# Optimization experiments

Measured on AMD Instinct MI355X. Metric: run time of the kernel, lower is better.

## Reference

```python
import jax, jax.numpy as jnp
import numpy as np

N_NODES = 100000
N_EDGES = 1600000
IN_FEATS = 128
HIDDEN = 128
NUM_CLASSES = 64


def setup_inputs() -> dict:
    key = jax.random.key(0)
    k1, k2, k3, k4, k5 = jax.random.split(key, 5)
    inputs = jax.random.normal(k1, (N_NODES, IN_FEATS), dtype=jnp.float32)
    src = jax.random.randint(k2, (N_EDGES,), 0, N_NODES, dtype=jnp.int32)
    dst = jax.random.randint(k3, (N_EDGES,), 0, N_NODES, dtype=jnp.int32)
    W1 = jax.random.normal(k4, (IN_FEATS, HIDDEN), dtype=jnp.float32) / np.sqrt(IN_FEATS)
    b1 = jnp.zeros((HIDDEN,), dtype=jnp.float32)
    W2 = jax.random.normal(k5, (HIDDEN, NUM_CLASSES), dtype=jnp.float32) / np.sqrt(HIDDEN)
    b2 = jnp.zeros((NUM_CLASSES,), dtype=jnp.float32)
    return {"inputs": inputs, "src": src, "dst": dst, "W1": W1, "b1": b1, "W2": W2, "b2": b2}


def _graph_conv(x, src, dst, W, b, n_nodes):
    # DGL GraphConv, norm='both': h = D_in^{-1/2} A D_out^{-1/2} x W + b
    ones = jnp.ones(src.shape[0], dtype=x.dtype)
    deg_out = jax.ops.segment_sum(ones, src, num_segments=n_nodes)
    deg_in = jax.ops.segment_sum(ones, dst, num_segments=n_nodes)
    norm_src = jax.lax.rsqrt(jnp.clip(deg_out, 1.0))  # [N]
    norm_dst = jax.lax.rsqrt(jnp.clip(deg_in, 1.0))   # [N]
    x = x * norm_src[:, None]
    msgs = x[src]                                      # [E, d] gather
    agg = jax.ops.segment_sum(msgs, dst, num_segments=n_nodes)  # [N, d] scatter-add
    agg = agg * norm_dst[:, None]
    return agg @ W + b


def reference(inputs, src, dst, W1, b1, W2, b2):
    n = inputs.shape[0]
    h = _graph_conv(inputs, src, dst, W1, b1, n)
    h = jax.nn.relu(h)
    h = _graph_conv(h, src, dst, W2, b2, n)
    return h
```

## Files before the change

kernel.cpp:

```cpp
#include <hip/hip_runtime.h>
#include <hip/hip_bf16.h>

#define N_FEATS_IN 128
#define BK_BITS 8
#define BK_SIZE 256
#define EPB 4096
#define MAXNB 512

typedef _Float16 h8 __attribute__((ext_vector_type(8)));
typedef float    f4v __attribute__((ext_vector_type(4)));
typedef float    f8v __attribute__((ext_vector_type(8)));

__device__ inline int wave_incl_scan(int v) {
    const int lane = threadIdx.x & 63;
    for (int off = 1; off < 64; off <<= 1) {
        int u = __shfl_up(v, off, 64);
        if (lane >= off) v += u;
    }
    return v;
}

__device__ inline int block_excl_scan(int s, int* ws, int* total) {
    const int lane = threadIdx.x & 63, wid = threadIdx.x >> 6;
    int inc = wave_incl_scan(s);
    if (lane == 63) ws[wid] = inc;
    __syncthreads();
    int woff = 0;
#pragma unroll
    for (int w = 0; w < 4; ++w) woff += (w < wid) ? ws[w] : 0;
    if (total) *total = ws[0] + ws[1] + ws[2] + ws[3];
    return woff + inc - s;
}

__global__ __launch_bounds__(256) void hist_kernel(
    const int* __restrict__ src, const int* __restrict__ dst,
    int* __restrict__ bh_d, int* __restrict__ bh_s,
    const float* __restrict__ W1, const float* __restrict__ W2,
    _Float16* __restrict__ wf1g, _Float16* __restrict__ wf2g,
    int E, int NB) {
    __shared__ int hd[MAXNB];
    __shared__ int hs[MAXNB];
    const int t = threadIdx.x;

    const int widx = blockIdx.x * 256 + t;
    if (widx < 128 * 128) {
        const int i = widx;
        const int k = i >> 7, c = i & 127;
        const int tt = c >> 4, s = k >> 5, q = (k >> 3) & 3, j = k & 7;
        wf1g[(((tt * 4 + s) * 4 + q) * 16 + (c & 15)) * 8 + j] =
            (_Float16)W1[i];
    } else if (widx < 128 * 128 + 128 * 64) {
        const int i = widx - 128 * 128;
        const int k = i >> 6, c = i & 63;
        const int tt = c >> 4, s = k >> 5, q = (k >> 3) & 3, j = k & 7;
        wf2g[(((tt * 4 + s) * 4 + q) * 16 + (c & 15)) * 8 + j] =
            (_Float16)W2[i];
    }

    for (int i = t; i < NB; i += 256) { hd[i] = 0; hs[i] = 0; }
    __syncthreads();
    const int base = blockIdx.x * EPB;
    const int end = min(base + EPB, E);
    for (int e = base + t; e < end; e += 256) {
        atomicAdd(&hd[dst[e] >> BK_BITS], 1);
        atomicAdd(&hs[src[e] >> BK_BITS], 1);
    }
    __syncthreads();
    for (int i = t; i < NB; i += 256) {
        bh_d[(size_t)blockIdx.x * NB + i] = hd[i];
        bh_s[(size_t)blockIdx.x * NB + i] = hs[i];
    }
}

__global__ __launch_bounds__(256) void colprefix2_kernel(
    int* __restrict__ bh_d, int* __restrict__ bh_s,
    int* __restrict__ tot_d, int* __restrict__ tot_s, int NBLK, int NB) {
    __shared__ int ws[4];
    const int b = blockIdx.x;
    const int t = threadIdx.x;
    int carry = 0;
    for (int base = 0; base < NBLK; base += 256) {
        const int r = base + t;
        const int v = (r < NBLK) ? bh_d[(size_t)r * NB + b] : 0;
        int total;
        const int e = block_excl_scan(v, ws, &total);
        if (r < NBLK) bh_d[(size_t)r * NB + b] = carry + e;
        carry += total;
        __syncthreads();
    }
    if (t == 0) tot_d[b] = carry;
    carry = 0;
    for (int base = 0; base < NBLK; base += 256) {
        const int r = base + t;
        const int v = (r < NBLK) ? bh_s[(size_t)r * NB + b] : 0;
        int total;
        const int e = block_excl_scan(v, ws, &total);
        if (r < NBLK) bh_s[(size_t)r * NB + b] = carry + e;
        carry += total;
        __syncthreads();
    }
    if (t == 0) tot_s[b] = carry;
}

__global__ __launch_bounds__(256) void bscan2_kernel(
    const int* __restrict__ tot_d, const int* __restrict__ tot_s,
    int* __restrict__ gb_d, int* __restrict__ gb_s,
    int* __restrict__ row_ptr, int NB, int N, int E) {
    __shared__ int ws[4];
    const int t = threadIdx.x;
    {
        const int a = (2 * t < NB) ? tot_d[2 * t] : 0;
        const int b = (2 * t + 1 < NB) ? tot_d[2 * t + 1] : 0;
        const int excl = block_excl_scan(a + b, ws, nullptr);
        if (2 * t < NB) gb_d[2 * t] = excl;
        if (2 * t + 1 < NB) gb_d[2 * t + 1] = excl + a;
    }
    __syncthreads();
    {
        const int a = (2 * t < NB) ? tot_s[2 * t] : 0;
        const int b = (2 * t + 1 < NB) ? tot_s[2 * t + 1] : 0;
        const int excl = block_excl_scan(a + b, ws, nullptr);
        if (2 * t < NB) gb_s[2 * t] = excl;
        if (2 * t + 1 < NB) gb_s[2 * t + 1] = excl + a;
    }
    if (t == 0) { gb_d[NB] = E; gb_s[NB] = E; row_ptr[N] = E; }
}

__global__ __launch_bounds__(256) void scatter2_kernel(
    const int* __restrict__ src, const int* __restrict__ dst,
    const int* __restrict__ bh_d, const int* __restrict__ bh_s,
    const int* __restrict__ gb_d, const int* __restrict__ gb_s,
    unsigned int* __restrict__ ebuf, unsigned char* __restrict__ sbuf,
    int E, int NB) {
    __shared__ int cd[MAXNB];
    __shared__ int cs[MAXNB];
    const int t = threadIdx.x;
    for (int i = t; i < NB; i += 256) {
        cd[i] = bh_d[(size_t)blockIdx.x * NB + i] + gb_d[i];
        cs[i] = bh_s[(size_t)blockIdx.x * NB + i] + gb_s[i];
    }
    __syncthreads();
    const int base = blockIdx.x * EPB;
    const int end = min(base + EPB, E);
    for (int e = base + t; e < end; e += 256) {
        const int d = dst[e];
        const int s = src[e];
        const int pd = atomicAdd(&cd[d >> BK_BITS], 1);
        ebuf[pd] = ((unsigned)s << 8) | (unsigned)(d & (BK_SIZE - 1));
        const int ps = atomicAdd(&cs[s >> BK_BITS], 1);
        sbuf[ps] = (unsigned char)(s & (BK_SIZE - 1));
    }
}

__global__ __launch_bounds__(256) void bucket_csr_kernel(
    const unsigned int* __restrict__ ebuf, const int* __restrict__ gb_d,
    const unsigned char* __restrict__ sbuf, const int* __restrict__ gb_s,
    int* __restrict__ row_ptr, float* __restrict__ norm_dst,
    float* __restrict__ norm_src, int* __restrict__ edge_src, int N) {
    __shared__ int cnt[BK_SIZE];
    __shared__ int lro[BK_SIZE];
    __shared__ int ws[4];
    const int b = blockIdx.x;
    const int t = threadIdx.x;
    const int beg = gb_d[b], end = gb_d[b + 1];
    const int node = b * BK_SIZE + t;

    cnt[t] = 0;
    __syncthreads();
    for (int j = beg + t; j < end; j += 256)
        atomicAdd(&cnt[ebuf[j] & (BK_SIZE - 1)], 1);
    __syncthreads();

    const int v = cnt[t];
    const int excl = block_excl_scan(v, ws, nullptr);
    lro[t] = beg + excl;
    if (node < N) {
        row_ptr[node] = beg + excl;
        norm_dst[node] = rsqrtf(fmaxf((float)v, 1.0f));
    }
    __syncthreads();
    cnt[t] = 0;
    __syncthreads();

    for (int j = beg + t; j < end; j += 256) {
        const unsigned int ed = ebuf[j];
        const int dl = ed & (BK_SIZE - 1);
        const int p = atomicAdd(&cnt[dl], 1);
        edge_src[lro[dl] + p] = (int)(ed >> 8);
    }

    __syncthreads();
    cnt[t] = 0;
    __syncthreads();
    const int sb = gb_s[b], se = gb_s[b + 1];
    for (int j = sb + t; j < se; j += 256)
        atomicAdd(&cnt[sbuf[j]], 1);
    __syncthreads();
    if (node < N)
        norm_src[node] = rsqrtf(fmaxf((float)cnt[t], 1.0f));
}

template <int OC, bool XHALF>
__global__ __launch_bounds__(256) void mfma_gemm_kernel(
    const void* __restrict__ Xv, const _Float16* __restrict__ Wg,
    const float* __restrict__ scale, _Float16* __restrict__ Y, int n) {
    constexpr int K = 128;
    constexpr int NT = OC / 16;
    constexpr int RPB = 128;
    __shared__ _Float16 Wf[NT * 4 * 64 * 8];

    const int tid = threadIdx.x;
    for (int i = tid * 8; i < K * OC; i += 256 * 8)
        *(h8*)&Wf[i] = *(const h8*)&Wg[i];
    __syncthreads();

    const int lane = tid & 63;
    const int wv = tid >> 6;
    const int m = lane & 15, q = lane >> 4;

#pragma unroll
    for (int it = 0; it < RPB / 64; ++it) {
        const int rbase = blockIdx.x * RPB + it * 64 + wv * 16;
        const int lrow = min(rbase + m, n - 1);

        h8 a[4];
        if constexpr (XHALF) {
            const _Float16* X = (const _Float16*)Xv;
            const _Float16* p = &X[(size_t)lrow * K + q * 8];
#pragma unroll
            for (int s = 0; s < 4; ++s) a[s] = *(const h8*)(p + s * 32);
        } else {
            const float* X = (const float*)Xv;
            const float* p = &X[(size_t)lrow * K + q * 8];
#pragma unroll
            for (int s = 0; s < 4; ++s) {
                const float4 u0 = *(const float4*)(p + s * 32);
                const float4 u1 = *(const float4*)(p + s * 32 + 4);
                h8 v;
                v[0] = (_Float16)u0.x; v[1] = (_Float16)u0.y;
                v[2] = (_Float16)u0.z; v[3] = (_Float16)u0.w;
                v[4] = (_Float16)u1.x; v[5] = (_Float16)u1.y;
                v[6] = (_Float16)u1.z; v[7] = (_Float16)u1.w;
                a[s] = v;
            }
        }

        f4v acc[NT];
#pragma unroll
        for (int t = 0; t < NT; ++t) acc[t] = (f4v)0.0f;

#pragma unroll
        for (int s = 0; s < 4; ++s) {
#pragma unroll
            for (int t = 0; t < NT; ++t) {
                const h8 b = *(const h8*)&Wf[((t * 4 + s) * 64 + lane) * 8];
                acc[t] = __builtin_amdgcn_mfma_f32_16x16x32_f16(
                    a[s], b, acc[t], 0, 0, 0);
            }
        }

#pragma unroll
        for (int r = 0; r < 4; ++r) {
            const int orow = rbase + q * 4 + r;
            if (orow < n) {
                const float sc = scale[orow];
#pragma unroll
                for (int t = 0; t < NT; ++t)
                    Y[(size_t)orow * OC + t * 16 + m] =
                        (_Float16)(acc[t][r] * sc);
            }
        }
    }
}

template <int FEAT, bool RELU, bool OUT_HALF>
__global__ __launch_bounds__(256) void gather_agg_kernel(
    const _Float16* __restrict__ T, const int* __restrict__ row_ptr,
    const int* __restrict__ edge_src, const float* __restrict__ norm_dst,
    const float* __restrict__ bias, void* __restrict__ outv, int n) {
    constexpr int TPN = FEAT / 8;
    constexpr int NPB = 256 / TPN;
    const int node = blockIdx.x * NPB + threadIdx.x / TPN;
    const int f8 = threadIdx.x % TPN;
    if (node >= n) return;
    const int beg = row_ptr[node];
    const int end = row_ptr[node + 1];
    const h8* T8 = (const h8*)T;

    f8v acc = (f8v)0.0f;
    int j = beg;
    for (; j + 7 < end; j += 8) {
        int s[8];
#pragma unroll
        for (int u = 0; u < 8; ++u) s[u] = edge_src[j + u];
        h8 a[8];
#pragma unroll
        for (int u = 0; u < 8; ++u) a[u] = T8[(size_t)s[u] * TPN + f8];
#pragma unroll
        for (int u = 0; u < 8; ++u)
            acc += __builtin_convertvector(a[u], f8v);
    }
    for (; j + 3 < end; j += 4) {
        int s[4];
#pragma unroll
        for (int u = 0; u < 4; ++u) s[u] = edge_src[j + u];
        h8 a[4];
#pragma unroll
        for (int u = 0; u < 4; ++u) a[u] = T8[(size_t)s[u] * TPN + f8];
#pragma unroll
        for (int u = 0; u < 4; ++u)
            acc += __builtin_convertvector(a[u], f8v);
    }
    for (; j < end; ++j)
        acc += __builtin_convertvector(T8[(size_t)edge_src[j] * TPN + f8], f8v);

    const float nd = norm_dst[node];
    float r[8];
#pragma unroll
    for (int k = 0; k < 8; ++k) {
        r[k] = acc[k] * nd + bias[f8 * 8 + k];
        if constexpr (RELU) r[k] = fmaxf(r[k], 0.0f);
    }

    if constexpr (OUT_HALF) {
        _Float16* out = (_Float16*)outv;
        h8 o;
#pragma unroll
        for (int k = 0; k < 8; ++k) o[k] = (_Float16)r[k];
        *(h8*)&out[(size_t)node * FEAT + f8 * 8] = o;
    } else {
        float* out = (float*)outv;
        float4 o0 = make_float4(r[0], r[1], r[2], r[3]);
        float4 o1 = make_float4(r[4], r[5], r[6], r[7]);
        *(float4*)&out[(size_t)node * FEAT + f8 * 8] = o0;
        *(float4*)&out[(size_t)node * FEAT + f8 * 8 + 4] = o1;
    }
}

template <int FEAT, int OC>
__global__ __launch_bounds__(256) void gather_gemm_kernel(
    const _Float16* __restrict__ T, const int* __restrict__ row_ptr,
    const int* __restrict__ edge_src, const float* __restrict__ norm_dst,
    const float* __restrict__ norm_src, const float* __restrict__ bias,
    const _Float16* __restrict__ Wg, _Float16* __restrict__ Y, int n) {
    constexpr int TPN = FEAT / 8;
    constexpr int NPB = 256 / TPN;
    constexpr int AP = FEAT + 8;
    __shared__ _Float16 Ah[NPB * AP];

    const int tid = threadIdx.x;
    const int node = blockIdx.x * NPB + tid / TPN;
    const int f8 = tid % TPN;
    const int nl = tid / TPN;
    const h8* T8 = (const h8*)T;

    float r[8];
    if (node < n) {
        const int beg = row_ptr[node];
        const int end = row_ptr[node + 1];
        f8v acc = (f8v)0.0f;
        int j = beg;
        for (; j + 7 < end; j += 8) {
            int s[8];
#pragma unroll
            for (int u = 0; u < 8; ++u) s[u] = edge_src[j + u];
            h8 a[8];
#pragma unroll
            for (int u = 0; u < 8; ++u) a[u] = T8[(size_t)s[u] * TPN + f8];
#pragma unroll
            for (int u = 0; u < 8; ++u)
                acc += __builtin_convertvector(a[u], f8v);
        }
        for (; j + 3 < end; j += 4) {
            int s[4];
#pragma unroll
            for (int u = 0; u < 4; ++u) s[u] = edge_src[j + u];
            h8 a[4];
#pragma unroll
            for (int u = 0; u < 4; ++u) a[u] = T8[(size_t)s[u] * TPN + f8];
#pragma unroll
            for (int u = 0; u < 4; ++u)
                acc += __builtin_convertvector(a[u], f8v);
        }
        for (; j < end; ++j)
            acc += __builtin_convertvector(T8[(size_t)edge_src[j] * TPN + f8],
                                           f8v);

        const float nd = norm_dst[node];
        const float ns = norm_src[node];
#pragma unroll
        for (int k = 0; k < 8; ++k) {
            float v = acc[k] * nd + bias[f8 * 8 + k];
            v = fmaxf(v, 0.0f);
            r[k] = v * ns;
        }
    } else {
#pragma unroll
        for (int k = 0; k < 8; ++k) r[k] = 0.0f;
    }

    {
        h8 av;
#pragma unroll
        for (int k = 0; k < 8; ++k) av[k] = (_Float16)r[k];
        *(h8*)&Ah[nl * AP + f8 * 8] = av;
    }
    __syncthreads();

    const int lane = tid & 63, w = tid >> 6;
    const int m = lane & 15, q = lane >> 4;
    f4v acc2 = (f4v)0.0f;
#pragma unroll
    for (int s = 0; s < 4; ++s) {
        const h8 a = *(const h8*)&Ah[m * AP + s * 32 + q * 8];
        const h8 b = *(const h8*)&Wg[((w * 4 + s) * 64 + lane) * 8];
        acc2 = __builtin_amdgcn_mfma_f32_16x16x32_f16(a, b, acc2, 0, 0, 0);
    }
#pragma unroll
    for (int rr = 0; rr < 4; ++rr) {
        const int orow = blockIdx.x * NPB + q * 4 + rr;
        if (orow < n)
            Y[(size_t)orow * OC + w * 16 + m] = (_Float16)acc2[rr];
    }
}

extern "C" void kernel_launch(void* const* d_in, const int* in_sizes, int n_in,
                              void* d_out, int out_size, void* d_ws, size_t ws_size,
                              hipStream_t stream) {
    const float* x   = (const float*)d_in[0];
    const int*   src = (const int*)d_in[1];
    const int*   dst = (const int*)d_in[2];
    const float* W1  = (const float*)d_in[3];
    const float* b1  = (const float*)d_in[4];
    const float* W2  = (const float*)d_in[5];
    const float* b2  = (const float*)d_in[6];
    float* out = (float*)d_out;

    const int N = in_sizes[0] / N_FEATS_IN;
    const int E = in_sizes[1];
    const int NB = (N + BK_SIZE - 1) / BK_SIZE;
    const int NBLK = (E + EPB - 1) / EPB;

    auto align4 = [](size_t w) { return (w + 3) & ~(size_t)3; };
    char* base = (char*)d_ws;
    size_t off = 0;
    auto take = [&](size_t words) {
        char* p = base + off * 4;
        off = align4(off + words);
        return p;
    };
    int*   tot_d    = (int*)take(NB);
    int*   tot_s    = (int*)take(NB);
    int*   gb_d     = (int*)take(NB + 1);
    int*   gb_s     = (int*)take(NB + 1);
    int*   bh_d     = (int*)take((size_t)NBLK * NB);
    int*   bh_s     = (int*)take((size_t)NBLK * NB);
    unsigned int*  ebuf = (unsigned int*)take(E);
    unsigned char* sbuf = (unsigned char*)take((E + 3) / 4);
    int*   row_ptr  = (int*)take(N + 1);
    int*   edge_src = (int*)take(E);
    float* norms    = (float*)take(2 * (size_t)N);
    _Float16* t1    = (_Float16*)take((size_t)N * 64);
    _Float16* t2    = (_Float16*)take((size_t)N * 32);
    _Float16* wf1g  = (_Float16*)take(128 * 128 / 2);
    _Float16* wf2g  = (_Float16*)take(128 * 64 / 2);
    float* norm_src = norms;
    float* norm_dst = norms + N;

    hist_kernel<<<NBLK, 256, 0, stream>>>(src, dst, bh_d, bh_s,
                                          W1, W2, wf1g, wf2g, E, NB);
    colprefix2_kernel<<<NB, 256, 0, stream>>>(bh_d, bh_s, tot_d, tot_s,
                                              NBLK, NB);
    bscan2_kernel<<<1, 256, 0, stream>>>(tot_d, tot_s, gb_d, gb_s, row_ptr,
                                         NB, N, E);
    scatter2_kernel<<<NBLK, 256, 0, stream>>>(src, dst, bh_d, bh_s, gb_d, gb_s,
                                              ebuf, sbuf, E, NB);
    bucket_csr_kernel<<<NB, 256, 0, stream>>>(ebuf, gb_d, sbuf, gb_s, row_ptr,
                                              norm_dst, norm_src, edge_src, N);

    mfma_gemm_kernel<128, false><<<(N + 127) / 128, 256, 0, stream>>>(
        x, wf1g, norm_src, t1, N);

    gather_gemm_kernel<128, 64><<<(N + 15) / 16, 256, 0, stream>>>(
        t1, row_ptr, edge_src, norm_dst, norm_src, b1, wf2g, t2, N);

    gather_agg_kernel<64, false, false><<<(N + 31) / 32, 256, 0, stream>>>(
        t2, row_ptr, edge_src, norm_dst, b2, out, N);
}
```

Before: 315.5 us.

## Replace bucketed two-level CSR build with global-atomic degree count and scan

```diff
diff --git a/kernel.cpp b/kernel.cpp
--- a/kernel.cpp
+++ b/kernel.cpp
@@ -2,10 +2,6 @@
 #include <hip/hip_bf16.h>
 
 #define N_FEATS_IN 128
-#define BK_BITS 8
-#define BK_SIZE 256
-#define EPB 4096
-#define MAXNB 512
 
 typedef _Float16 h8 __attribute__((ext_vector_type(8)));
 typedef float    f4v __attribute__((ext_vector_type(4)));
@@ -32,172 +28,97 @@
     return woff + inc - s;
 }
 
-__global__ __launch_bounds__(256) void hist_kernel(
-    const int* __restrict__ src, const int* __restrict__ dst,
-    int* __restrict__ bh_d, int* __restrict__ bh_s,
+__global__ __launch_bounds__(256) void zswz_kernel(
+    int* __restrict__ deg_in, int* __restrict__ deg_out,
     const float* __restrict__ W1, const float* __restrict__ W2,
-    _Float16* __restrict__ wf1g, _Float16* __restrict__ wf2g,
-    int E, int NB) {
-    __shared__ int hd[MAXNB];
-    __shared__ int hs[MAXNB];
-    const int t = threadIdx.x;
-
-    const int widx = blockIdx.x * 256 + t;
-    if (widx < 128 * 128) {
-        const int i = widx;
+    _Float16* __restrict__ wf1g, _Float16* __restrict__ wf2g, int N) {
+    const int g = blockIdx.x * 256 + threadIdx.x;
+    if (g < N) { deg_in[g] = 0; deg_out[g] = 0; }
+    if (g < 128 * 128) {
+        const int i = g;
         const int k = i >> 7, c = i & 127;
         const int tt = c >> 4, s = k >> 5, q = (k >> 3) & 3, j = k & 7;
         wf1g[(((tt * 4 + s) * 4 + q) * 16 + (c & 15)) * 8 + j] =
             (_Float16)W1[i];
-    } else if (widx < 128 * 128 + 128 * 64) {
-        const int i = widx - 128 * 128;
+    } else if (g < 128 * 128 + 128 * 64) {
+        const int i = g - 128 * 128;
         const int k = i >> 6, c = i & 63;
         const int tt = c >> 4, s = k >> 5, q = (k >> 3) & 3, j = k & 7;
         wf2g[(((tt * 4 + s) * 4 + q) * 16 + (c & 15)) * 8 + j] =
             (_Float16)W2[i];
     }
-
-    for (int i = t; i < NB; i += 256) { hd[i] = 0; hs[i] = 0; }
-    __syncthreads();
-    const int base = blockIdx.x * EPB;
-    const int end = min(base + EPB, E);
-    for (int e = base + t; e < end; e += 256) {
-        atomicAdd(&hd[dst[e] >> BK_BITS], 1);
-        atomicAdd(&hs[src[e] >> BK_BITS], 1);
-    }
-    __syncthreads();
-    for (int i = t; i < NB; i += 256) {
-        bh_d[(size_t)blockIdx.x * NB + i] = hd[i];
-        bh_s[(size_t)blockIdx.x * NB + i] = hs[i];
-    }
-}
-
-__global__ __launch_bounds__(256) void colprefix2_kernel(
-    int* __restrict__ bh_d, int* __restrict__ bh_s,
-    int* __restrict__ tot_d, int* __restrict__ tot_s, int NBLK, int NB) {
-    __shared__ int ws[4];
-    const int b = blockIdx.x;
-    const int t = threadIdx.x;
-    int carry = 0;
-    for (int base = 0; base < NBLK; base += 256) {
-        const int r = base + t;
-        const int v = (r < NBLK) ? bh_d[(size_t)r * NB + b] : 0;
-        int total;
-        const int e = block_excl_scan(v, ws, &total);
-        if (r < NBLK) bh_d[(size_t)r * NB + b] = carry + e;
-        carry += total;
-        __syncthreads();
-    }
-    if (t == 0) tot_d[b] = carry;
-    carry = 0;
-    for (int base = 0; base < NBLK; base += 256) {
-        const int r = base + t;
-        const int v = (r < NBLK) ? bh_s[(size_t)r * NB + b] : 0;
-        int total;
-        const int e = block_excl_scan(v, ws, &total);
-        if (r < NBLK) bh_s[(size_t)r * NB + b] = carry + e;
-        carry += total;
-        __syncthreads();
-    }
-    if (t == 0) tot_s[b] = carry;
-}
-
-__global__ __launch_bounds__(256) void bscan2_kernel(
-    const int* __restrict__ tot_d, const int* __restrict__ tot_s,
-    int* __restrict__ gb_d, int* __restrict__ gb_s,
-    int* __restrict__ row_ptr, int NB, int N, int E) {
+}
+
+__global__ __launch_bounds__(256) void deg_kernel(
+    const int* __restrict__ src, const int* __restrict__ dst,
+    int* __restrict__ deg_in, int* __restrict__ deg_out, int E) {
+    const int stride = gridDim.x * 256;
+    for (int e = blockIdx.x * 256 + threadIdx.x; e < E; e += stride) {
+        atomicAdd(&deg_in[dst[e]], 1);
+        atomicAdd(&deg_out[src[e]], 1);
+    }
+}
+
+__global__ __launch_bounds__(256) void scanA_kernel(
+    const int* __restrict__ deg, int* __restrict__ rp,
+    int* __restrict__ part, int N) {
     __shared__ int ws[4];
     const int t = threadIdx.x;
-    {
-        const int a = (2 * t < NB) ? tot_d[2 * t] : 0;
-        const int b = (2 * t + 1 < NB) ? tot_d[2 * t + 1] : 0;
-        const int excl = block_excl_scan(a + b, ws, nullptr);
-        if (2 * t < NB) gb_d[2 * t] = excl;
-        if (2 * t + 1 < NB) gb_d[2 * t + 1] = excl + a;
-    }
-    __syncthreads();
-    {
-        const int a = (2 * t < NB) ? tot_s[2 * t] : 0;
-        const int b = (2 * t + 1 < NB) ? tot_s[2 * t + 1] : 0;
-        const int excl = block_excl_scan(a + b, ws, nullptr);
-        if (2 * t < NB) gb_s[2 * t] = excl;
-        if (2 * t + 1 < NB) gb_s[2 * t + 1] = excl + a;
-    }
-    if (t == 0) { gb_d[NB] = E; gb_s[NB] = E; row_ptr[N] = E; }
-}
-
-__global__ __launch_bounds__(256) void scatter2_kernel(
+    const int i0 = (blockIdx.x * 256 + t) * 4;
+    int d0 = 0, d1 = 0, d2 = 0, d3 = 0;
+    if (i0 + 3 < N) {
+        const int4 v = *(const int4*)&deg[i0];
+        d0 = v.x; d1 = v.y; d2 = v.z; d3 = v.w;
+    } else {
+        if (i0 < N) d0 = deg[i0];
+        if (i0 + 1 < N) d1 = deg[i0 + 1];
+        if (i0 + 2 < N) d2 = deg[i0 + 2];
+        if (i0 + 3 < N) d3 = deg[i0 + 3];
+    }
+    int tot;
+    int r = block_excl_scan(d0 + d1 + d2 + d3, ws, &tot);
+    if (i0 < N) rp[i0] = r; r += d0;
+    if (i0 + 1 < N) rp[i0 + 1] = r; r += d1;
+    if (i0 + 2 < N) rp[i0 + 2] = r; r += d2;
+    if (i0 + 3 < N) rp[i0 + 3] = r;
+    if (t == 0) part[blockIdx.x] = tot;
+}
+
+__global__ __launch_bounds__(256) void scanB_kernel(
+    int* __restrict__ part, int nbs) {
+    __shared__ int ws[4];
+    const int t = threadIdx.x;
+    const int v = (t < nbs) ? part[t] : 0;
+    const int e = block_excl_scan(v, ws, nullptr);
+    if (t < nbs) part[t] = e;
+}
+
+__global__ __launch_bounds__(256) void scanC_kernel(
+    int* __restrict__ rp, int* __restrict__ cur,
+    const int* __restrict__ part,
+    const int* __restrict__ deg_in, const int* __restrict__ deg_out,
+    float* __restrict__ norm_dst, float* __restrict__ norm_src,
+    int N, int E) {
+    const int i = blockIdx.x * 256 + threadIdx.x;
+    if (i < N) {
+        const int r = rp[i] + part[i >> 10];
+        rp[i] = r;
+        cur[i] = r;
+        norm_dst[i] = rsqrtf(fmaxf((float)deg_in[i], 1.0f));
+        norm_src[i] = rsqrtf(fmaxf((float)deg_out[i], 1.0f));
+    }
+    if (i == 0) rp[N] = E;
+}
+
+__global__ __launch_bounds__(256) void scatter_kernel(
     const int* __restrict__ src, const int* __restrict__ dst,
-    const int* __restrict__ bh_d, const int* __restrict__ bh_s,
-    const int* __restrict__ gb_d, const int* __restrict__ gb_s,
-    unsigned int* __restrict__ ebuf, unsigned char* __restrict__ sbuf,
-    int E, int NB) {
-    __shared__ int cd[MAXNB];
-    __shared__ int cs[MAXNB];
-    const int t = threadIdx.x;
-    for (int i = t; i < NB; i += 256) {
-        cd[i] = bh_d[(size_t)blockIdx.x * NB + i] + gb_d[i];
-        cs[i] = bh_s[(size_t)blockIdx.x * NB + i] + gb_s[i];
-    }
-    __syncthreads();
-    const int base = blockIdx.x * EPB;
-    const int end = min(base + EPB, E);
-    for (int e = base + t; e < end; e += 256) {
+    int* __restrict__ cur, int* __restrict__ edge_src, int E) {
+    const int stride = gridDim.x * 256;
+    for (int e = blockIdx.x * 256 + threadIdx.x; e < E; e += stride) {
         const int d = dst[e];
-        const int s = src[e];
-        const int pd = atomicAdd(&cd[d >> BK_BITS], 1);
-        ebuf[pd] = ((unsigned)s << 8) | (unsigned)(d & (BK_SIZE - 1));
-        const int ps = atomicAdd(&cs[s >> BK_BITS], 1);
-        sbuf[ps] = (unsigned char)(s & (BK_SIZE - 1));
-    }
-}
-
-__global__ __launch_bounds__(256) void bucket_csr_kernel(
-    const unsigned int* __restrict__ ebuf, const int* __restrict__ gb_d,
-    const unsigned char* __restrict__ sbuf, const int* __restrict__ gb_s,
-    int* __restrict__ row_ptr, float* __restrict__ norm_dst,
-    float* __restrict__ norm_src, int* __restrict__ edge_src, int N) {
-    __shared__ int cnt[BK_SIZE];
-    __shared__ int lro[BK_SIZE];
-    __shared__ int ws[4];
-    const int b = blockIdx.x;
-    const int t = threadIdx.x;
-    const int beg = gb_d[b], end = gb_d[b + 1];
-    const int node = b * BK_SIZE + t;
-
-    cnt[t] = 0;
-    __syncthreads();
-    for (int j = beg + t; j < end; j += 256)
-        atomicAdd(&cnt[ebuf[j] & (BK_SIZE - 1)], 1);
-    __syncthreads();
-
-    const int v = cnt[t];
-    const int excl = block_excl_scan(v, ws, nullptr);
-    lro[t] = beg + excl;
-    if (node < N) {
-        row_ptr[node] = beg + excl;
-        norm_dst[node] = rsqrtf(fmaxf((float)v, 1.0f));
-    }
-    __syncthreads();
-    cnt[t] = 0;
-    __syncthreads();
-
-    for (int j = beg + t; j < end; j += 256) {
-        const unsigned int ed = ebuf[j];
-        const int dl = ed & (BK_SIZE - 1);
-        const int p = atomicAdd(&cnt[dl], 1);
-        edge_src[lro[dl] + p] = (int)(ed >> 8);
-    }
-
-    __syncthreads();
-    cnt[t] = 0;
-    __syncthreads();
-    const int sb = gb_s[b], se = gb_s[b + 1];
-    for (int j = sb + t; j < se; j += 256)
-        atomicAdd(&cnt[sbuf[j]], 1);
-    __syncthreads();
-    if (node < N)
-        norm_src[node] = rsqrtf(fmaxf((float)cnt[t], 1.0f));
+        const int pos = atomicAdd(&cur[d], 1);
+        edge_src[pos] = src[e];
+    }
 }
 
 template <int OC, bool XHALF>
@@ -438,8 +359,7 @@
 
     const int N = in_sizes[0] / N_FEATS_IN;
     const int E = in_sizes[1];
-    const int NB = (N + BK_SIZE - 1) / BK_SIZE;
-    const int NBLK = (E + EPB - 1) / EPB;
+    const int NBS = (N + 1023) / 1024;
 
     auto align4 = [](size_t w) { return (w + 3) & ~(size_t)3; };
     char* base = (char*)d_ws;
@@ -449,14 +369,10 @@
         off = align4(off + words);
         return p;
     };
-    int*   tot_d    = (int*)take(NB);
-    int*   tot_s    = (int*)take(NB);
-    int*   gb_d     = (int*)take(NB + 1);
-    int*   gb_s     = (int*)take(NB + 1);
-    int*   bh_d     = (int*)take((size_t)NBLK * NB);
-    int*   bh_s     = (int*)take((size_t)NBLK * NB);
-    unsigned int*  ebuf = (unsigned int*)take(E);
-    unsigned char* sbuf = (unsigned char*)take((E + 3) / 4);
+    int*   deg_in   = (int*)take(N);
+    int*   deg_out  = (int*)take(N);
+    int*   cur      = (int*)take(N);
+    int*   part     = (int*)take(256);
     int*   row_ptr  = (int*)take(N + 1);
     int*   edge_src = (int*)take(E);
     float* norms    = (float*)take(2 * (size_t)N);
@@ -467,16 +383,14 @@
     float* norm_src = norms;
     float* norm_dst = norms + N;
 
-    hist_kernel<<<NBLK, 256, 0, stream>>>(src, dst, bh_d, bh_s,
-                                          W1, W2, wf1g, wf2g, E, NB);
-    colprefix2_kernel<<<NB, 256, 0, stream>>>(bh_d, bh_s, tot_d, tot_s,
-                                              NBLK, NB);
-    bscan2_kernel<<<1, 256, 0, stream>>>(tot_d, tot_s, gb_d, gb_s, row_ptr,
-                                         NB, N, E);
-    scatter2_kernel<<<NBLK, 256, 0, stream>>>(src, dst, bh_d, bh_s, gb_d, gb_s,
-                                              ebuf, sbuf, E, NB);
-    bucket_csr_kernel<<<NB, 256, 0, stream>>>(ebuf, gb_d, sbuf, gb_s, row_ptr,
-                                              norm_dst, norm_src, edge_src, N);
+    zswz_kernel<<<(N + 255) / 256, 256, 0, stream>>>(
+        deg_in, deg_out, W1, W2, wf1g, wf2g, N);
+    deg_kernel<<<2048, 256, 0, stream>>>(src, dst, deg_in, deg_out, E);
+    scanA_kernel<<<NBS, 256, 0, stream>>>(deg_in, row_ptr, part, N);
+    scanB_kernel<<<1, 256, 0, stream>>>(part, NBS);
+    scanC_kernel<<<(N + 255) / 256, 256, 0, stream>>>(
+        row_ptr, cur, part, deg_in, deg_out, norm_dst, norm_src, N, E);
+    scatter_kernel<<<2048, 256, 0, stream>>>(src, dst, cur, edge_src, E);
 
     mfma_gemm_kernel<128, false><<<(N + 127) / 128, 256, 0, stream>>>(
         x, wf1g, norm_src, t1, N);
```

Measured after the change: 499.8 us. 1.58x slower.
